# Optimization experiments

Measured on AMD Instinct MI355X. Metric: run time of the kernel, lower is better.

## Reference

```python
import jax, jax.numpy as jnp
import numpy as np

BN_EPS = 1e-5
MIN_LENGTH = 10
HIDDEN = 256


def _conv(x, w, stride):
    # x: [N,C,H,W], w: [O,I,3,3], SAME-ish padding 1
    return jax.lax.conv_general_dilated(
        x, w, (stride, stride), [(1, 1), (1, 1)],
        dimension_numbers=("NCHW", "OIHW", "NCHW"))


def _bn_relu(x, g, b, m, v):
    # eval-mode BatchNorm2d followed by ReLU, folded into scale/shift
    inv = g / jnp.sqrt(v + BN_EPS)
    return jax.nn.relu(x * inv[None, :, None, None] + (b - m * inv)[None, :, None, None])


def setup_inputs() -> dict:
    key = jax.random.key(0)
    ks = jax.random.split(key, 16)
    B, S, C, H, W = 16, 64, 3, 64, 64
    d = {"imgs": jax.random.normal(ks[0], (B, S, C, H, W), dtype=jnp.float32)}
    # conv stack: (out_ch, in_ch, stride)
    specs = [(16, 3, 2), (16, 16, 1), (32, 16, 2), (32, 32, 1), (64, 32, 2), (64, 64, 1)]
    for i, (o, ic, _s) in enumerate(specs):
        d[f"w{i}"] = jax.random.normal(ks[1 + i], (o, ic, 3, 3), dtype=jnp.float32) * 0.05
        d[f"g{i}"] = jnp.ones((o,), jnp.float32)
        d[f"b{i}"] = jnp.zeros((o,), jnp.float32)
        d[f"m{i}"] = jnp.zeros((o,), jnp.float32)
        d[f"v{i}"] = jnp.ones((o,), jnp.float32)
    in_dim = 64 * 8 * 8  # plane3 * 8 * 8
    d["w_ih"] = jax.random.normal(ks[8], (4 * HIDDEN, in_dim), dtype=jnp.float32) * 0.02
    d["w_hh"] = jax.random.normal(ks[9], (4 * HIDDEN, HIDDEN), dtype=jnp.float32) * 0.05
    d["b_ih"] = jnp.zeros((4 * HIDDEN,), jnp.float32)
    d["b_hh"] = jnp.zeros((4 * HIDDEN,), jnp.float32)
    d["cls_w"] = jax.random.normal(ks[10], (1, HIDDEN), dtype=jnp.float32) * 0.05
    d["cls_b"] = jnp.zeros((1,), jnp.float32)
    return d


def reference(imgs, w0, g0, b0, m0, v0, w1, g1, b1, m1, v1, w2, g2, b2, m2, v2,
              w3, g3, b3, m3, v3, w4, g4, b4, m4, v4, w5, g5, b5, m5, v5,
              w_ih, w_hh, b_ih, b_hh, cls_w, cls_b):
    B, S, C, H, W = imgs.shape
    x = imgs.reshape(B * S, C, H, W)
    layers = [(w0, g0, b0, m0, v0, 2), (w1, g1, b1, m1, v1, 1),
              (w2, g2, b2, m2, v2, 2), (w3, g3, b3, m3, v3, 1),
              (w4, g4, b4, m4, v4, 2), (w5, g5, b5, m5, v5, 1)]
    for w, g, b, m, v, s in layers:
        x = _bn_relu(_conv(x, w, s), g, b, m, v)
    # [B*S, 64, 8, 8] -> [S, B, 4096]
    feats = x.reshape(B, S, -1).transpose(1, 0, 2)

    def step(carry, x_t):
        h, c = carry
        gates = x_t @ w_ih.T + b_ih + h @ w_hh.T + b_hh
        i, f, g, o = jnp.split(gates, 4, axis=-1)
        c = jax.nn.sigmoid(f) * c + jax.nn.sigmoid(i) * jnp.tanh(g)
        h = jax.nn.sigmoid(o) * jnp.tanh(c)
        return (h, c), h

    h0 = jnp.zeros((B, HIDDEN), feats.dtype)
    c0 = jnp.zeros((B, HIDDEN), feats.dtype)
    _, hs = jax.lax.scan(step, (h0, c0), feats)  # [S, B, 256]
    kept = hs[MIN_LENGTH + 1:]                    # [S-11, B, 256]
    out = jnp.tanh(kept @ cls_w.T + cls_b)        # [S-11, B, 1]
    return out.transpose(1, 0, 2)                 # [B, S-11, 1]
```

## Files before the change

### kernel.cpp

```cpp
#include <hip/hip_runtime.h>
#include <cmath>


typedef __attribute__((ext_vector_type(8))) __bf16 bf16x8;
typedef __attribute__((ext_vector_type(4))) float f32x4;

__device__ __forceinline__ float sigmoidf_(float x) { return 1.f / (1.f + expf(-x)); }

__device__ __forceinline__ float fsig_(float x) {
  return __builtin_amdgcn_rcpf(1.f + __expf(-x));
}
__device__ __forceinline__ float ftanh_(float x) {
  float xc = fminf(fmaxf(x, -15.f), 15.f);
  float e = __expf(2.f * xc);
  return (e - 1.f) * __builtin_amdgcn_rcpf(e + 1.f);
}

__device__ __forceinline__ unsigned short f2bf(float f) {
  unsigned u = __float_as_uint(f);
  unsigned r = (u + 0x7fffu + ((u >> 16) & 1u)) >> 16;
  return (unsigned short)r;
}
__device__ __forceinline__ float bf2f(unsigned short h) {
  return __uint_as_float(((unsigned)h) << 16);
}

struct FoldPack {
  const float *w[6], *g[6], *b[6], *m[6], *v[6];
  float *wf[6], *bias[6];
  int oc[6], ic[6];
};

__global__ __launch_bounds__(256) void fold_all(FoldPack p) {
  const int layer = blockIdx.y;
  const int OC = p.oc[layer], IC = p.ic[layer];
  const int total = OC * IC * 9;
  const float* w = p.w[layer];
  float* wf = p.wf[layer];
  for (int i = blockIdx.x * 256 + threadIdx.x; i < total; i += gridDim.x * 256) {
    int oc = i / (IC * 9);
    int r  = i % (IC * 9);
    int ic = r / 9;
    int k  = r % 9;
    int ky = k / 3, kx = k % 3;
    float inv = p.g[layer][oc] / sqrtf(p.v[layer][oc] + 1e-5f);
    wf[(((ic * 3 + ky) * OC) + oc) * 4 + kx] = w[i] * inv;
  }
  if (blockIdx.x == 0) {
    int i = threadIdx.x;
    if (i < OC) {
      float inv = p.g[layer][i] / sqrtf(p.v[layer][i] + 1e-5f);
      p.bias[layer][i] = p.b[layer][i] - p.m[layer][i] * inv;
    }
  }
}

struct PackPack {
  const float *w[5], *g[5], *v[5];
  unsigned short *wh[5], *wl[5];
  int ic[5], oc[5], kg[5], kreal[5];
};

__global__ __launch_bounds__(256) void pack_w(PackPack p) {
  const int layer = blockIdx.y;
  const int IC = p.ic[layer], KG = p.kg[layer], K = p.kreal[layer];
  const int MT = p.oc[layer] / 16;
  const int total = MT * KG * 512;
  for (int i = blockIdx.x * 256 + threadIdx.x; i < total; i += gridDim.x * 256) {
    int j = i & 7;
    int lane = (i >> 3) & 63;
    int gmt = i >> 9;
    int m = (gmt / KG) * 16 + (lane & 15);
    int k = 32 * (gmt % KG) + 8 * (lane >> 4) + j;
    float val = 0.f;
    if (k < K) {
      int tap = k / IC, ic = k % IC;
      int ky = tap / 3, kx = tap % 3;
      float inv = p.g[layer][m] / sqrtf(p.v[layer][m] + 1e-5f);
      val = p.w[layer][((m * IC + ic) * 3 + ky) * 3 + kx] * inv;
    }
    unsigned short h = f2bf(val);
    p.wh[layer][i] = h;
    p.wl[layer][i] = f2bf(val - bf2f(h));
  }
}

template<int IC, int OC, int IH, int IW, int STRIDE, int TPOS, int SPLITY,
         int ICS, int MINW>
__global__ __launch_bounds__(256, MINW) void conv_bn_relu(
    const float* __restrict__ in, const float* __restrict__ wf,
    const float* __restrict__ bias, float* __restrict__ out)
{
  constexpr int OH = IH / STRIDE, OW = IW / STRIDE;
  constexpr int OHB = OH / SPLITY;
  constexpr int RIH = (SPLITY == 1) ? (IH + 2) : ((OHB - 1) * STRIDE + 3);
  constexpr int PIW = IW + 4;
  constexpr int PLANE = RIH * PIW;
  constexpr int NPOS = OHB * OW;
  constexpr int WPOS = NPOS / TPOS;
  constexpr int SLOT = WPOS * ICS;
  constexpr int GROUPS = 256 / SLOT;
  constexpr int TOC = OC / GROUPS;
  constexpr int CH = IC / ICS;
  constexpr int SPAN = (TPOS - 1) * STRIDE + 3;
  constexpr int NW = (SPAN + 3) / 4;
  constexpr int XSLOTS = OW / TPOS;
  static_assert(SLOT % 64 == 0 && GROUPS * SLOT == 256 && GROUPS * TOC == OC, "tiling");

  __shared__ float s_in[IC * PLANE];

  const int tid = threadIdx.x;
  const int n     = (SPLITY == 1) ? blockIdx.x : blockIdx.x / SPLITY;
  const int split = (SPLITY == 1) ? 0 : blockIdx.x % SPLITY;
  const int ry0 = split * OHB;
  const int r0  = ry0 * STRIDE - 1;

  for (int i = tid; i < IC * PLANE / 4; i += 256)
    ((float4*)s_in)[i] = float4{0.f, 0.f, 0.f, 0.f};
  __syncthreads();

  constexpr int ROWF4 = IW / 4;
  constexpr int NSTG = IC * RIH * ROWF4;
  for (int i = tid; i < NSTG; i += 256) {
    int rw  = i % ROWF4;
    int t   = i / ROWF4;
    int row = t % RIH;
    int ic  = t / RIH;
    int giy = r0 + row;
    if (giy >= 0 && giy < IH) {
      float4 v = *(const float4*)(in + ((size_t)(n * IC + ic) * IH + giy) * IW + rw * 4);
      float* dst = &s_in[(ic * RIH + row) * PIW + 1 + rw * 4];
      dst[0] = v.x; dst[1] = v.y; dst[2] = v.z; dst[3] = v.w;
    }
  }
  __syncthreads();

  const int group  = tid / SLOT;
  const int sl     = tid % SLOT;
  const int icq    = sl / WPOS;
  const int worker = sl % WPOS;
  const int oy  = worker / XSLOTS;
  const int ox0 = (worker % XSLOTS) * TPOS;
  const int xb  = ox0 * STRIDE;

  const int oc0u = __builtin_amdgcn_readfirstlane(group * TOC);
  const float4* wg = (const float4*)wf + oc0u;

  float acc[TOC][TPOS];
  #pragma unroll
  for (int a = 0; a < TOC; ++a)
    #pragma unroll
    for (int p = 0; p < TPOS; ++p) acc[a][p] = 0.f;

  for (int icl = 0; icl < CH; ++icl) {
    const int ic = icq * CH + icl;
    const float* sI = &s_in[ic * PLANE];
    #pragma unroll
    for (int ky = 0; ky < 3; ++ky) {
      float row[NW * 4];
      {
        const float4* rp = (const float4*)&sI[(oy * STRIDE + ky) * PIW + xb];
        #pragma unroll
        for (int w = 0; w < NW; ++w) {
          float4 t4 = rp[w];
          row[4*w+0] = t4.x; row[4*w+1] = t4.y;
          row[4*w+2] = t4.z; row[4*w+3] = t4.w;
        }
      }
      const float4* wrow = wg + (ic * 3 + ky) * OC;
      #pragma unroll
      for (int oc = 0; oc < TOC; ++oc) {
        float4 w4 = wrow[oc];
        #pragma unroll
        for (int p = 0; p < TPOS; ++p)
          acc[oc][p] = fmaf(row[p * STRIDE + 0], w4.x,
                       fmaf(row[p * STRIDE + 1], w4.y,
                       fmaf(row[p * STRIDE + 2], w4.z, acc[oc][p])));
      }
    }
  }

  #pragma unroll
  for (int d = WPOS; d < SLOT; d <<= 1)
    #pragma unroll
    for (int oc = 0; oc < TOC; ++oc)
      #pragma unroll
      for (int p = 0; p < TPOS; ++p)
        acc[oc][p] += __shfl_xor(acc[oc][p], d);

  if (icq == 0) {
    float* outN = out + (size_t)n * (OC * OH * OW);
    #pragma unroll
    for (int oc = 0; oc < TOC; ++oc) {
      const float bb = bias[oc0u + oc];
      float* op = outN + ((size_t)(oc0u + oc) * OH + (ry0 + oy)) * OW + ox0;
      #pragma unroll
      for (int vq = 0; vq < TPOS / 4; ++vq) {
        float4 val;
        val.x = fmaxf(acc[oc][vq*4+0] + bb, 0.f);
        val.y = fmaxf(acc[oc][vq*4+1] + bb, 0.f);
        val.z = fmaxf(acc[oc][vq*4+2] + bb, 0.f);
        val.w = fmaxf(acc[oc][vq*4+3] + bb, 0.f);
        *(float4*)(op + vq * 4) = val;
      }
    }
  }
}

template<int IC, int OC, int IH, int IW, int STRIDE, int SPLITY, int KG, int ZROW>
__global__ __launch_bounds__(256, 2) void conv_mfma(
    const float* __restrict__ in, const unsigned short* __restrict__ Ah,
    const unsigned short* __restrict__ Al, const float* __restrict__ bias,
    float* __restrict__ out)
{
  constexpr int OH = IH / STRIDE, OW = IW / STRIDE;
  constexpr int OHB = OH / SPLITY;
  constexpr int N = OHB * OW;
  constexpr int NT = N / 16;
  constexpr int NTW = NT / 4;
  constexpr int MT = OC / 16;
  constexpr int ICP = IC + 8;
  constexpr int PW = IW + 3;
  constexpr int PH = (OHB - 1) * STRIDE + 3 + ZROW;
  constexpr int SZ = ((PH * PW * ICP + 7) / 8) * 8;
  static_assert(NT % 4 == 0, "nt");

  __shared__ unsigned short s_h[SZ];
  __shared__ unsigned short s_l[SZ];

  const int tid = threadIdx.x;
  const int n     = (SPLITY == 1) ? blockIdx.x : blockIdx.x / SPLITY;
  const int split = (SPLITY == 1) ? 0 : blockIdx.x % SPLITY;
  const int y0 = split * OHB;
  const int r0 = y0 * STRIDE - 1;

  for (int i = tid * 8; i < SZ; i += 2048) {
    *(int4*)&s_h[i] = int4{0, 0, 0, 0};
    *(int4*)&s_l[i] = int4{0, 0, 0, 0};
  }
  __syncthreads();

  constexpr int ROWF4 = IW / 4;
  for (int i = tid; i < IC * PH * ROWF4; i += 256) {
    int rw  = i % ROWF4;
    int t   = i / ROWF4;
    int row = t % PH;
    int ic  = t / PH;
    int giy = r0 + row;
    if (giy >= 0 && giy < IH) {
      float4 v = *(const float4*)(in + ((size_t)(n * IC + ic) * IH + giy) * IW + rw * 4);
      int base = (row * PW + rw * 4 + 1) * ICP + ic;
      float vv[4] = {v.x, v.y, v.z, v.w};
      #pragma unroll
      for (int e = 0; e < 4; ++e) {
        unsigned short h = f2bf(vv[e]);
        s_h[base + e * ICP] = h;
        s_l[base + e * ICP] = f2bf(vv[e] - bf2f(h));
      }
    }
  }
  __syncthreads();

  const int wave = tid >> 6;
  const int lane = tid & 63;
  const int l16  = lane & 15;
  const int quad = lane >> 4;

  f32x4 acc[MT][NTW];
  #pragma unroll
  for (int mt = 0; mt < MT; ++mt)
    #pragma unroll
    for (int nt = 0; nt < NTW; ++nt) acc[mt][nt] = f32x4{0.f, 0.f, 0.f, 0.f};

  for (int g = 0; g < KG; ++g) {
    const int k0 = 32 * g + 8 * quad;
    const int tap = k0 / IC;
    const int ic0 = k0 % IC;
    const int ky = tap / 3;
    const int kx = tap - ky * 3;
    bf16x8 afh[MT], afl[MT];
    #pragma unroll
    for (int mt = 0; mt < MT; ++mt) {
      size_t wo = ((size_t)(mt * KG + g) * 64 + lane) * 8;
      afh[mt] = __builtin_bit_cast(bf16x8, *(const int4*)(Ah + wo));
      afl[mt] = __builtin_bit_cast(bf16x8, *(const int4*)(Al + wo));
    }
    #pragma unroll
    for (int nt = 0; nt < NTW; ++nt) {
      int p = (wave * NTW + nt) * 16 + l16;
      int py = p / OW, px = p % OW;
      int addr = ((py * STRIDE + ky) * PW + px * STRIDE + kx) * ICP + ic0;
      bf16x8 bh = __builtin_bit_cast(bf16x8, *(const int4*)&s_h[addr]);
      bf16x8 bl = __builtin_bit_cast(bf16x8, *(const int4*)&s_l[addr]);
      #pragma unroll
      for (int mt = 0; mt < MT; ++mt) {
        acc[mt][nt] = __builtin_amdgcn_mfma_f32_16x16x32_bf16(afh[mt], bh, acc[mt][nt], 0, 0, 0);
        acc[mt][nt] = __builtin_amdgcn_mfma_f32_16x16x32_bf16(afh[mt], bl, acc[mt][nt], 0, 0, 0);
        acc[mt][nt] = __builtin_amdgcn_mfma_f32_16x16x32_bf16(afl[mt], bh, acc[mt][nt], 0, 0, 0);
      }
    }
  }

  #pragma unroll
  for (int mt = 0; mt < MT; ++mt)
    #pragma unroll
    for (int nt = 0; nt < NTW; ++nt) {
      int p = (wave * NTW + nt) * 16 + l16;
      int py = p / OW, px = p % OW;
      #pragma unroll
      for (int r = 0; r < 4; ++r) {
        int oc = mt * 16 + quad * 4 + r;
        float v = acc[mt][nt][r] + bias[oc];
        out[((size_t)(n * OC + oc) * OH + y0 + py) * OW + px] = fmaxf(v, 0.f);
      }
    }
}

__global__ __launch_bounds__(256) void split_a(
    const float* __restrict__ feats, unsigned short* __restrict__ ah,
    unsigned short* __restrict__ al)
{
  int i4 = blockIdx.x * 256 + threadIdx.x;
  int e = i4 * 4;
  int n = e >> 12;
  int k = e & 4095;
  int r = (n & 63) * 16 + (n >> 6);
  float4 v = ((const float4*)feats)[i4];
  ushort4 h, l;
  h.x = f2bf(v.x); l.x = f2bf(v.x - bf2f(h.x));
  h.y = f2bf(v.y); l.y = f2bf(v.y - bf2f(h.y));
  h.z = f2bf(v.z); l.z = f2bf(v.z - bf2f(h.z));
  h.w = f2bf(v.w); l.w = f2bf(v.w - bf2f(h.w));
  *(ushort4*)(ah + (size_t)r * 4096 + k) = h;
  *(ushort4*)(al + (size_t)r * 4096 + k) = l;
}

__global__ __launch_bounds__(256) void split_b(
    const float* __restrict__ w_ih, unsigned short* __restrict__ bh,
    unsigned short* __restrict__ bl)
{
  int i4 = blockIdx.x * 256 + threadIdx.x;
  float4 v = ((const float4*)w_ih)[i4];
  ushort4 h, l;
  h.x = f2bf(v.x); l.x = f2bf(v.x - bf2f(h.x));
  h.y = f2bf(v.y); l.y = f2bf(v.y - bf2f(h.y));
  h.z = f2bf(v.z); l.z = f2bf(v.z - bf2f(h.z));
  h.w = f2bf(v.w); l.w = f2bf(v.w - bf2f(h.w));
  ((ushort4*)bh)[i4] = h;
  ((ushort4*)bl)[i4] = l;
}

__global__ __launch_bounds__(256) void mfma_xg(
    const unsigned short* __restrict__ Ah, const unsigned short* __restrict__ Al,
    const unsigned short* __restrict__ Bh, const unsigned short* __restrict__ Bl,
    float* __restrict__ part)
{
  __shared__ unsigned short s_ah[128 * 40];
  __shared__ unsigned short s_al[128 * 40];
  __shared__ unsigned short s_bh[128 * 40];
  __shared__ unsigned short s_bl[128 * 40];

  const int tid = threadIdx.x;
  const int col0 = blockIdx.x * 128;
  const int row0 = blockIdx.y * 128;
  const int kbase = blockIdx.z * 512;
  float* outp = part + (size_t)blockIdx.z * 1048576;

  const int wave = tid >> 6;
  const int lane = tid & 63;
  const int wr = wave >> 1, wc = wave & 1;
  const int quad = lane >> 4;
  const int l16 = lane & 15;

  f32x4 acc[4][4];
  #pragma unroll
  for (int i = 0; i < 4; ++i)
    #pragma unroll
    for (int j = 0; j < 4; ++j) acc[i][j] = f32x4{0.f, 0.f, 0.f, 0.f};

  for (int step = 0; step < 16; ++step) {
    const int koff = kbase + step * 32;
    #pragma unroll
    for (int c = tid; c < 512; c += 256) {
      int row = c >> 2, kc = (c & 3) * 8;
      int4 va = *(const int4*)(Ah + (size_t)(row0 + row) * 4096 + koff + kc);
      int4 vb = *(const int4*)(Al + (size_t)(row0 + row) * 4096 + koff + kc);
      int4 vc = *(const int4*)(Bh + (size_t)(col0 + row) * 4096 + koff + kc);
      int4 vd = *(const int4*)(Bl + (size_t)(col0 + row) * 4096 + koff + kc);
      *(int4*)&s_ah[row * 40 + kc] = va;
      *(int4*)&s_al[row * 40 + kc] = vb;
      *(int4*)&s_bh[row * 40 + kc] = vc;
      *(int4*)&s_bl[row * 40 + kc] = vd;
    }
    __syncthreads();

    bf16x8 arh[4], arl[4];
    #pragma unroll
    for (int i = 0; i < 4; ++i) {
      int m = wr * 64 + i * 16 + l16;
      arh[i] = __builtin_bit_cast(bf16x8, *(const int4*)&s_ah[m * 40 + quad * 8]);
      arl[i] = __builtin_bit_cast(bf16x8, *(const int4*)&s_al[m * 40 + quad * 8]);
    }
    #pragma unroll
    for (int j = 0; j < 4; ++j) {
      int nn = wc * 64 + j * 16 + l16;
      bf16x8 brh = __builtin_bit_cast(bf16x8, *(const int4*)&s_bh[nn * 40 + quad * 8]);
      bf16x8 brl = __builtin_bit_cast(bf16x8, *(const int4*)&s_bl[nn * 40 + quad * 8]);
      #pragma unroll
      for (int i = 0; i < 4; ++i) {
        acc[i][j] = __builtin_amdgcn_mfma_f32_16x16x32_bf16(arh[i], brh, acc[i][j], 0, 0, 0);
        acc[i][j] = __builtin_amdgcn_mfma_f32_16x16x32_bf16(arh[i], brl, acc[i][j], 0, 0, 0);
        acc[i][j] = __builtin_amdgcn_mfma_f32_16x16x32_bf16(arl[i], brh, acc[i][j], 0, 0, 0);
      }
    }
    __syncthreads();
  }

  #pragma unroll
  for (int i = 0; i < 4; ++i)
    #pragma unroll
    for (int j = 0; j < 4; ++j) {
      int row = row0 + wr * 64 + i * 16 + quad * 4;
      int col = col0 + wc * 64 + j * 16 + l16;
      #pragma unroll
      for (int r = 0; r < 4; ++r)
        outp[(size_t)(row + r) * 1024 + col] = acc[i][j][r];
    }
}

__global__ __launch_bounds__(256) void reduce_xg(
    const float* __restrict__ p, const float* __restrict__ b_ih,
    const float* __restrict__ b_hh, float* __restrict__ xg)
{
  int i = blockIdx.x * 256 + threadIdx.x;
  float4 s = {0.f, 0.f, 0.f, 0.f};
  #pragma unroll
  for (int z = 0; z < 8; ++z) {
    float4 a = ((const float4*)p)[(size_t)z * 262144 + i];
    s.x += a.x; s.y += a.y; s.z += a.z; s.w += a.w;
  }
  int cb = i & 255;
  float4 bi = ((const float4*)b_ih)[cb];
  float4 bh = ((const float4*)b_hh)[cb];
  float4 o;
  o.x = s.x + bi.x + bh.x;
  o.y = s.y + bi.y + bh.y;
  o.z = s.z + bi.z + bh.z;
  o.w = s.w + bi.w + bh.w;
  ((float4*)xg)[i] = o;
}

__global__ __launch_bounds__(1024, 4) void lstm_kernel(
    const float* __restrict__ xg, const float* __restrict__ w_hh,
    float* __restrict__ hs, unsigned long long* __restrict__ hpair)
{
  const int b = blockIdx.x & 15;
  const int g = blockIdx.x >> 4;
  const int tid = threadIdx.x;
  const int r = tid >> 2;
  const int q = tid & 3;
  const int gate = r >> 6;
  const int jl = r & 63;
  const int j = g * 64 + jl;

  float4 wv[16];
  {
    const float4* wrow = (const float4*)(w_hh + ((size_t)(gate * 256 + j)) * 256 + q * 64);
    #pragma unroll
    for (int k = 0; k < 16; ++k) wv[k] = wrow[k];
  }
  #pragma unroll
  for (int k = 0; k < 16; ++k)
    asm volatile("" : "+v"(wv[k].x), "+v"(wv[k].y), "+v"(wv[k].z), "+v"(wv[k].w));

  __shared__ float s_h[4 * 72];
  __shared__ float s_gates[4][64];
  float c_reg = 0.f;

  for (int s = 0; s < 64; ++s) {
    float xv = 0.f;
    if (q == 0) xv = xg[(size_t)(s * 16 + b) * 1024 + gate * 256 + j];
    float gv = 0.f;
    if (s > 0) {
      if (tid < 256) {
        const unsigned long long* src = hpair + ((size_t)(s - 1) * 16 + b) * 256 + tid;
        unsigned long long pv;
        do {
          pv = __hip_atomic_load(src, __ATOMIC_RELAXED, __HIP_MEMORY_SCOPE_AGENT);
        } while ((unsigned int)(pv >> 32) != (unsigned int)s);
        s_h[(tid >> 6) * 72 + (tid & 63)] = __uint_as_float((unsigned int)pv);
      }
      __syncthreads();
      const float4* hp = (const float4*)&s_h[q * 72];
      float p = 0.f;
      #pragma unroll
      for (int k = 0; k < 16; ++k) {
        float4 h4 = hp[k];
        p = fmaf(h4.x, wv[k].x, p);
        p = fmaf(h4.y, wv[k].y, p);
        p = fmaf(h4.z, wv[k].z, p);
        p = fmaf(h4.w, wv[k].w, p);
      }
      p += __shfl_xor(p, 1);
      p += __shfl_xor(p, 2);
      gv = p;
    }
    if (q == 0) s_gates[gate][jl] = gv + xv;
    __syncthreads();
    if (tid < 64) {
      float gi = s_gates[0][tid], gf = s_gates[1][tid];
      float gg = s_gates[2][tid], go = s_gates[3][tid];
      float cn = fsig_(gf) * c_reg + fsig_(gi) * ftanh_(gg);
      c_reg = cn;
      float hv = fsig_(go) * ftanh_(cn);
      hs[(size_t)s * 4096 + b * 256 + g * 64 + tid] = hv;
      unsigned long long pv =
          ((unsigned long long)(unsigned int)(s + 1) << 32) | __float_as_uint(hv);
      __hip_atomic_store(hpair + ((size_t)s * 16 + b) * 256 + g * 64 + tid, pv,
                         __ATOMIC_RELAXED, __HIP_MEMORY_SCOPE_AGENT);
    }
  }
}

__global__ __launch_bounds__(64) void cls_kernel(
    const float* __restrict__ hs, const float* __restrict__ cw,
    const float* __restrict__ cb, float* __restrict__ out)
{
  const int id = blockIdx.x;
  const int b = id / 53;
  const int t = id % 53;
  const int s = 11 + t;
  const int lane = threadIdx.x;
  float4 hv = ((const float4*)(hs + (size_t)s * 4096 + b * 256))[lane];
  float4 wv = ((const float4*)cw)[lane];
  float p = hv.x * wv.x + hv.y * wv.y + hv.z * wv.z + hv.w * wv.w;
  #pragma unroll
  for (int off = 32; off >= 1; off >>= 1) p += __shfl_xor(p, off);
  if (lane == 0) out[id] = tanhf(p + cb[0]);
}

extern "C" void kernel_launch(void* const* d_in, const int* in_sizes, int n_in,
                              void* d_out, int out_size, void* d_ws, size_t ws_size,
                              hipStream_t stream)
{
  (void)in_sizes; (void)n_in; (void)out_size; (void)ws_size;
  const float* imgs = (const float*)d_in[0];
  const float* w_ih  = (const float*)d_in[31];
  const float* w_hh  = (const float*)d_in[32];
  const float* b_ih  = (const float*)d_in[33];
  const float* b_hh  = (const float*)d_in[34];
  const float* cls_w = (const float*)d_in[35];
  const float* cls_b = (const float*)d_in[36];
  float* out = (float*)d_out;

  float* ws   = (float*)d_ws;
  float* actA = ws;
  float* actB = actA + 16777216;
  float* xg   = actB + 16777216;
  float* hs   = xg + 1048576;
  unsigned long long* hpair = (unsigned long long*)(hs + 262144);
  float* wfp  = hs + 262144 + 524288;
  static const int ocs[6] = {16, 16, 32, 32, 64, 64};
  static const int ics[6] = {3, 16, 16, 32, 32, 64};
  float* wf[6];
  size_t off = 0;
  for (int i = 0; i < 6; ++i) { wf[i] = wfp + off; off += (size_t)ocs[i] * ics[i] * 12; }
  float* biasp = wfp + off;
  float* bias[6];
  for (int i = 0; i < 6; ++i) bias[i] = biasp + i * 64;

  static const int psz[5] = {2560, 5120, 9216, 18432, 36864};
  unsigned short* WH = (unsigned short*)(biasp + 6 * 64);
  unsigned short* WL = WH + 72192;
  unsigned short *wh[5], *wl[5];
  {
    int o = 0;
    for (int i = 0; i < 5; ++i) { wh[i] = WH + o; wl[i] = WL + o; o += psz[i]; }
  }

  float* partials = actA;
  unsigned short* Ah = (unsigned short*)(actA + 8388608);
  unsigned short* Al = Ah + 4194304;
  unsigned short* Bh = Al + 4194304;
  unsigned short* Bl = Bh + 4194304;

  FoldPack fp;
  for (int i = 0; i < 6; ++i) {
    fp.w[i] = (const float*)d_in[1 + 5*i];
    fp.g[i] = (const float*)d_in[2 + 5*i];
    fp.b[i] = (const float*)d_in[3 + 5*i];
    fp.m[i] = (const float*)d_in[4 + 5*i];
    fp.v[i] = (const float*)d_in[5 + 5*i];
    fp.wf[i] = wf[i];
    fp.bias[i] = bias[i];
    fp.oc[i] = ocs[i];
    fp.ic[i] = ics[i];
  }
  fold_all<<<dim3(8, 6), 256, 0, stream>>>(fp);

  PackPack pp;
  static const int kgs[5] = {5, 5, 9, 9, 18};
  static const int krs[5] = {144, 144, 288, 288, 576};
  for (int i = 0; i < 5; ++i) {
    pp.w[i] = (const float*)d_in[1 + 5*(i+1)];
    pp.g[i] = (const float*)d_in[2 + 5*(i+1)];
    pp.v[i] = (const float*)d_in[5 + 5*(i+1)];
    pp.wh[i] = wh[i];
    pp.wl[i] = wl[i];
    pp.ic[i] = ics[i+1];
    pp.oc[i] = ocs[i+1];
    pp.kg[i] = kgs[i];
    pp.kreal[i] = krs[i];
  }
  pack_w<<<dim3(36, 5), 256, 0, stream>>>(pp);

  conv_bn_relu<3, 16, 64, 64, 2, 4, 2, 1, 4><<<2048, 256, 0, stream>>>(imgs, wf[0], bias[0], actA);
  conv_mfma<16, 16, 32, 32, 1, 4, 5, 1><<<4096, 256, 0, stream>>>(actA, wh[0], wl[0], bias[1], actB);
  conv_mfma<16, 32, 32, 32, 2, 4, 5, 1><<<4096, 256, 0, stream>>>(actB, wh[1], wl[1], bias[2], actA);
  conv_mfma<32, 32, 16, 16, 1, 1, 9, 0><<<1024, 256, 0, stream>>>(actA, wh[2], wl[2], bias[3], actB);
  conv_mfma<32, 64, 16, 16, 2, 1, 9, 0><<<1024, 256, 0, stream>>>(actB, wh[3], wl[3], bias[4], actA);
  conv_mfma<64, 64,  8,  8, 1, 1, 18, 0><<<1024, 256, 0, stream>>>(actA, wh[4], wl[4], bias[5], actB);

  split_a<<<4096, 256, 0, stream>>>(actB, Ah, Al);
  split_b<<<4096, 256, 0, stream>>>(w_ih, Bh, Bl);
  mfma_xg<<<dim3(8, 8, 8), 256, 0, stream>>>(Ah, Al, Bh, Bl, partials);
  reduce_xg<<<1024, 256, 0, stream>>>(partials, b_ih, b_hh, xg);
  lstm_kernel<<<64, 1024, 0, stream>>>(xg, w_hh, hs, hpair);
  cls_kernel<<<848, 64, 0, stream>>>(hs, cls_w, cls_b, out);
}
```

Baseline: 490.4 us.

## Rewrite LSTM recurrence using bf16x3 MFMA over hidden-unit blocks

Measured after the change: 741.5 us. 51.2% more time.

```diff
diff --git a/kernel.cpp b/kernel.cpp
--- a/kernel.cpp
+++ b/kernel.cpp
@@ -85,6 +85,25 @@
   }
 }
 
+__global__ __launch_bounds__(256) void pack_whh(
+    const float* __restrict__ w_hh, unsigned short* __restrict__ ph,
+    unsigned short* __restrict__ pl)
+{
+  int i = blockIdx.x * 256 + threadIdx.x;
+  int e = i & 7;
+  int lane = (i >> 3) & 63;
+  int g = (i >> 9) & 7;
+  int gw = i >> 12;
+  int gate = gw & 3;
+  int bk = gw >> 2;
+  int j = bk * 16 + (lane & 15);
+  int k = 32 * g + 8 * (lane >> 4) + e;
+  float val = w_hh[((size_t)(gate * 256 + j)) * 256 + k];
+  unsigned short h = f2bf(val);
+  ph[i] = h;
+  pl[i] = f2bf(val - bf2f(h));
+}
+
 template<int IC, int OC, int IH, int IW, int STRIDE, int TPOS, int SPLITY,
          int ICS, int MINW>
 __global__ __launch_bounds__(256, MINW) void conv_bn_relu(
@@ -450,75 +469,89 @@
   ((float4*)xg)[i] = o;
 }
 
-__global__ __launch_bounds__(1024, 4) void lstm_kernel(
-    const float* __restrict__ xg, const float* __restrict__ w_hh,
-    float* __restrict__ hs, unsigned long long* __restrict__ hpair)
-{
-  const int b = blockIdx.x & 15;
-  const int g = blockIdx.x >> 4;
+__global__ __launch_bounds__(256, 1) void lstm_mfma(
+    const float* __restrict__ xg, const unsigned short* __restrict__ Wh,
+    const unsigned short* __restrict__ Wl, float* __restrict__ hs,
+    unsigned long long* __restrict__ hpair)
+{
+  const int bk = blockIdx.x;
   const int tid = threadIdx.x;
-  const int r = tid >> 2;
-  const int q = tid & 3;
-  const int gate = r >> 6;
-  const int jl = r & 63;
-  const int j = g * 64 + jl;
-
-  float4 wv[16];
-  {
-    const float4* wrow = (const float4*)(w_hh + ((size_t)(gate * 256 + j)) * 256 + q * 64);
-    #pragma unroll
-    for (int k = 0; k < 16; ++k) wv[k] = wrow[k];
-  }
-  #pragma unroll
-  for (int k = 0; k < 16; ++k)
-    asm volatile("" : "+v"(wv[k].x), "+v"(wv[k].y), "+v"(wv[k].z), "+v"(wv[k].w));
-
-  __shared__ float s_h[4 * 72];
-  __shared__ float s_gates[4][64];
+  const int wave = tid >> 6;
+  const int lane = tid & 63;
+  const int l16 = lane & 15;
+  const int quad = lane >> 4;
+
+  bf16x8 ah[8], al[8];
+  #pragma unroll
+  for (int g = 0; g < 8; ++g) {
+    size_t o = (((size_t)(bk * 4 + wave) * 8 + g) * 64 + lane) * 8;
+    ah[g] = __builtin_bit_cast(bf16x8, *(const int4*)(Wh + o));
+    al[g] = __builtin_bit_cast(bf16x8, *(const int4*)(Wl + o));
+  }
+
+  __shared__ unsigned short s_hh[16][264];
+  __shared__ unsigned short s_hl[16][264];
+  __shared__ float s_g[4][16][17];
+
+  const int cb = tid >> 4;
+  const int cj = tid & 15;
+  const int jglob = bk * 16 + cj;
   float c_reg = 0.f;
 
   for (int s = 0; s < 64; ++s) {
-    float xv = 0.f;
-    if (q == 0) xv = xg[(size_t)(s * 16 + b) * 1024 + gate * 256 + j];
-    float gv = 0.f;
+    const float* xp = xg + (size_t)(s * 16 + cb) * 1024 + jglob;
+    float xv0 = xp[0];
+    float xv1 = xp[256];
+    float xv2 = xp[512];
+    float xv3 = xp[768];
+
+    f32x4 acc = f32x4{0.f, 0.f, 0.f, 0.f};
     if (s > 0) {
-      if (tid < 256) {
-        const unsigned long long* src = hpair + ((size_t)(s - 1) * 16 + b) * 256 + tid;
-        unsigned long long pv;
-        do {
-          pv = __hip_atomic_load(src, __ATOMIC_RELAXED, __HIP_MEMORY_SCOPE_AGENT);
-        } while ((unsigned int)(pv >> 32) != (unsigned int)s);
-        s_h[(tid >> 6) * 72 + (tid & 63)] = __uint_as_float((unsigned int)pv);
+      const unsigned long long* src = hpair + (size_t)(s - 1) * 4096 + tid;
+      unsigned long long pv[16];
+      #pragma unroll
+      for (int i = 0; i < 16; ++i)
+        pv[i] = __hip_atomic_load(src + i * 256, __ATOMIC_RELAXED,
+                                  __HIP_MEMORY_SCOPE_AGENT);
+      #pragma unroll
+      for (int i = 0; i < 16; ++i) {
+        while ((unsigned)(pv[i] >> 32) != (unsigned)s)
+          pv[i] = __hip_atomic_load(src + i * 256, __ATOMIC_RELAXED,
+                                    __HIP_MEMORY_SCOPE_AGENT);
+        float hv = __uint_as_float((unsigned)pv[i]);
+        unsigned short hh = f2bf(hv);
+        s_hh[i][tid] = hh;
+        s_hl[i][tid] = f2bf(hv - bf2f(hh));
       }
       __syncthreads();
-      const float4* hp = (const float4*)&s_h[q * 72];
-      float p = 0.f;
-      #pragma unroll
-      for (int k = 0; k < 16; ++k) {
-        float4 h4 = hp[k];
-        p = fmaf(h4.x, wv[k].x, p);
-        p = fmaf(h4.y, wv[k].y, p);
-        p = fmaf(h4.z, wv[k].z, p);
-        p = fmaf(h4.w, wv[k].w, p);
-      }
-      p += __shfl_xor(p, 1);
-      p += __shfl_xor(p, 2);
-      gv = p;
-    }
-    if (q == 0) s_gates[gate][jl] = gv + xv;
+
+      #pragma unroll
+      for (int g = 0; g < 8; ++g) {
+        const int off = 32 * g + quad * 8;
+        bf16x8 bh = __builtin_bit_cast(bf16x8, *(const int4*)&s_hh[l16][off]);
+        bf16x8 bl = __builtin_bit_cast(bf16x8, *(const int4*)&s_hl[l16][off]);
+        acc = __builtin_amdgcn_mfma_f32_16x16x32_bf16(ah[g], bh, acc, 0, 0, 0);
+        acc = __builtin_amdgcn_mfma_f32_16x16x32_bf16(ah[g], bl, acc, 0, 0, 0);
+        acc = __builtin_amdgcn_mfma_f32_16x16x32_bf16(al[g], bh, acc, 0, 0, 0);
+      }
+    }
+    #pragma unroll
+    for (int r = 0; r < 4; ++r)
+      s_g[wave][quad * 4 + r][l16] = acc[r];
     __syncthreads();
-    if (tid < 64) {
-      float gi = s_gates[0][tid], gf = s_gates[1][tid];
-      float gg = s_gates[2][tid], go = s_gates[3][tid];
-      float cn = fsig_(gf) * c_reg + fsig_(gi) * ftanh_(gg);
-      c_reg = cn;
-      float hv = fsig_(go) * ftanh_(cn);
-      hs[(size_t)s * 4096 + b * 256 + g * 64 + tid] = hv;
-      unsigned long long pv =
-          ((unsigned long long)(unsigned int)(s + 1) << 32) | __float_as_uint(hv);
-      __hip_atomic_store(hpair + ((size_t)s * 16 + b) * 256 + g * 64 + tid, pv,
-                         __ATOMIC_RELAXED, __HIP_MEMORY_SCOPE_AGENT);
-    }
+
+    float gi = s_g[0][cj][cb] + xv0;
+    float gf = s_g[1][cj][cb] + xv1;
+    float gg = s_g[2][cj][cb] + xv2;
+    float go = s_g[3][cj][cb] + xv3;
+    float cn = fsig_(gf) * c_reg + fsig_(gi) * ftanh_(gg);
+    c_reg = cn;
+    float hv = fsig_(go) * ftanh_(cn);
+    hs[(size_t)s * 4096 + cb * 256 + jglob] = hv;
+    unsigned long long opv =
+        ((unsigned long long)(unsigned)(s + 1) << 32) | __float_as_uint(hv);
+    __hip_atomic_store(hpair + (size_t)s * 4096 + cb * 256 + jglob, opv,
+                       __ATOMIC_RELAXED, __HIP_MEMORY_SCOPE_AGENT);
   }
 }
 
@@ -584,6 +617,9 @@
   unsigned short* Bh = Al + 4194304;
   unsigned short* Bl = Bh + 4194304;
 
+  unsigned short* WHH_H = (unsigned short*)actB;
+  unsigned short* WHH_L = WHH_H + 262144;
+
   FoldPack fp;
   for (int i = 0; i < 6; ++i) {
     fp.w[i] = (const float*)d_in[1 + 5*i];
@@ -623,8 +659,9 @@
 
   split_a<<<4096, 256, 0, stream>>>(actB, Ah, Al);
   split_b<<<4096, 256, 0, stream>>>(w_ih, Bh, Bl);
+  pack_whh<<<1024, 256, 0, stream>>>(w_hh, WHH_H, WHH_L);
   mfma_xg<<<dim3(8, 8, 8), 256, 0, stream>>>(Ah, Al, Bh, Bl, partials);
   reduce_xg<<<1024, 256, 0, stream>>>(partials, b_ih, b_hh, xg);
-  lstm_kernel<<<64, 1024, 0, stream>>>(xg, w_hh, hs, hpair);
+  lstm_mfma<<<16, 256, 0, stream>>>(xg, WHH_H, WHH_L, hs, hpair);
   cls_kernel<<<848, 64, 0, stream>>>(hs, cls_w, cls_b, out);
 }
```

## Split LSTM recurrence across 256 small blocks with parallel gate activations

Applied to the files above, without the earlier changes.

Measured after the change: 497.9 us. No clear change (+1.5%).

```diff
diff --git a/kernel.cpp b/kernel.cpp
--- a/kernel.cpp
+++ b/kernel.cpp
@@ -450,18 +450,18 @@
   ((float4*)xg)[i] = o;
 }
 
-__global__ __launch_bounds__(1024, 4) void lstm_kernel(
+__global__ __launch_bounds__(256, 1) void lstm_kernel(
     const float* __restrict__ xg, const float* __restrict__ w_hh,
     float* __restrict__ hs, unsigned long long* __restrict__ hpair)
 {
   const int b = blockIdx.x & 15;
-  const int g = blockIdx.x >> 4;
+  const int c = blockIdx.x >> 4;
   const int tid = threadIdx.x;
   const int r = tid >> 2;
   const int q = tid & 3;
-  const int gate = r >> 6;
-  const int jl = r & 63;
-  const int j = g * 64 + jl;
+  const int gate = r >> 4;
+  const int jl = r & 15;
+  const int j = c * 16 + jl;
 
   float4 wv[16];
   {
@@ -469,12 +469,9 @@
     #pragma unroll
     for (int k = 0; k < 16; ++k) wv[k] = wrow[k];
   }
-  #pragma unroll
-  for (int k = 0; k < 16; ++k)
-    asm volatile("" : "+v"(wv[k].x), "+v"(wv[k].y), "+v"(wv[k].z), "+v"(wv[k].w));
-
-  __shared__ float s_h[4 * 72];
-  __shared__ float s_gates[4][64];
+
+  __shared__ float s_h[4][68];
+  __shared__ float s_gates[4][17];
   float c_reg = 0.f;
 
   for (int s = 0; s < 64; ++s) {
@@ -482,41 +479,50 @@
     if (q == 0) xv = xg[(size_t)(s * 16 + b) * 1024 + gate * 256 + j];
     float gv = 0.f;
     if (s > 0) {
-      if (tid < 256) {
-        const unsigned long long* src = hpair + ((size_t)(s - 1) * 16 + b) * 256 + tid;
-        unsigned long long pv;
-        do {
-          pv = __hip_atomic_load(src, __ATOMIC_RELAXED, __HIP_MEMORY_SCOPE_AGENT);
-        } while ((unsigned int)(pv >> 32) != (unsigned int)s);
-        s_h[(tid >> 6) * 72 + (tid & 63)] = __uint_as_float((unsigned int)pv);
-      }
+      const unsigned long long* src = hpair + ((size_t)(s - 1) * 16 + b) * 256 + tid;
+      unsigned long long pv;
+      do {
+        pv = __hip_atomic_load(src, __ATOMIC_RELAXED, __HIP_MEMORY_SCOPE_AGENT);
+      } while ((unsigned int)(pv >> 32) != (unsigned int)s);
+      s_h[tid >> 6][tid & 63] = __uint_as_float((unsigned int)pv);
       __syncthreads();
-      const float4* hp = (const float4*)&s_h[q * 72];
-      float p = 0.f;
-      #pragma unroll
-      for (int k = 0; k < 16; ++k) {
-        float4 h4 = hp[k];
-        p = fmaf(h4.x, wv[k].x, p);
-        p = fmaf(h4.y, wv[k].y, p);
-        p = fmaf(h4.z, wv[k].z, p);
-        p = fmaf(h4.w, wv[k].w, p);
-      }
+      const float4* hp = (const float4*)&s_h[q][0];
+      float p0 = 0.f, p1 = 0.f;
+      #pragma unroll
+      for (int kc = 0; kc < 16; kc += 2) {
+        float4 ha = hp[kc];
+        float4 hb = hp[kc + 1];
+        p0 = fmaf(ha.x, wv[kc].x, p0);
+        p0 = fmaf(ha.y, wv[kc].y, p0);
+        p0 = fmaf(ha.z, wv[kc].z, p0);
+        p0 = fmaf(ha.w, wv[kc].w, p0);
+        p1 = fmaf(hb.x, wv[kc + 1].x, p1);
+        p1 = fmaf(hb.y, wv[kc + 1].y, p1);
+        p1 = fmaf(hb.z, wv[kc + 1].z, p1);
+        p1 = fmaf(hb.w, wv[kc + 1].w, p1);
+      }
+      float p = p0 + p1;
       p += __shfl_xor(p, 1);
       p += __shfl_xor(p, 2);
       gv = p;
-    }
-    if (q == 0) s_gates[gate][jl] = gv + xv;
+    } else {
+      __syncthreads();
+    }
+    if (q == 0) {
+      float pre = gv + xv;
+      s_gates[gate][jl] = (gate == 2) ? ftanh_(pre) : fsig_(pre);
+    }
     __syncthreads();
-    if (tid < 64) {
-      float gi = s_gates[0][tid], gf = s_gates[1][tid];
-      float gg = s_gates[2][tid], go = s_gates[3][tid];
-      float cn = fsig_(gf) * c_reg + fsig_(gi) * ftanh_(gg);
+    if (tid < 16) {
+      float si = s_gates[0][tid], sf = s_gates[1][tid];
+      float tg = s_gates[2][tid], so = s_gates[3][tid];
+      float cn = sf * c_reg + si * tg;
       c_reg = cn;
-      float hv = fsig_(go) * ftanh_(cn);
-      hs[(size_t)s * 4096 + b * 256 + g * 64 + tid] = hv;
+      float hv = so * ftanh_(cn);
+      hs[(size_t)s * 4096 + b * 256 + c * 16 + tid] = hv;
       unsigned long long pv =
           ((unsigned long long)(unsigned int)(s + 1) << 32) | __float_as_uint(hv);
-      __hip_atomic_store(hpair + ((size_t)s * 16 + b) * 256 + g * 64 + tid, pv,
+      __hip_atomic_store(hpair + ((size_t)s * 16 + b) * 256 + c * 16 + tid, pv,
                          __ATOMIC_RELAXED, __HIP_MEMORY_SCOPE_AGENT);
     }
   }
@@ -625,6 +631,6 @@
   split_b<<<4096, 256, 0, stream>>>(w_ih, Bh, Bl);
   mfma_xg<<<dim3(8, 8, 8), 256, 0, stream>>>(Ah, Al, Bh, Bl, partials);
   reduce_xg<<<1024, 256, 0, stream>>>(partials, b_ih, b_hh, xg);
-  lstm_kernel<<<64, 1024, 0, stream>>>(xg, w_hh, hs, hpair);
+  lstm_kernel<<<256, 256, 0, stream>>>(xg, w_hh, hs, hpair);
   cls_kernel<<<848, 64, 0, stream>>>(hs, cls_w, cls_b, out);
 }
```
